# Optimization experiments

Hardware: AMD Instinct MI355X
Metric: run time of the kernel (lower is better)

## Reference

```python
import jax, jax.numpy as jnp
import numpy as np
import math

H = 32      # num attention heads
KV = 8      # num key/value heads
D = 64      # head dim
ROPE_BASE = 10000.0


def _rope_cos_sin(seq_len, dtype):
    inv_freq = 1.0 / (ROPE_BASE ** (jnp.arange(0, D, 2, dtype=jnp.float32) / D))
    t = jnp.arange(seq_len, dtype=jnp.float32)
    freqs = jnp.einsum('i,j->ij', t, inv_freq)          # [S, D/2]
    emb = jnp.concatenate([freqs, freqs], axis=-1)       # [S, D]
    return jnp.cos(emb).astype(dtype)[None, None], jnp.sin(emb).astype(dtype)[None, None]


def _rotate_half(x):
    x1, x2 = x[..., : D // 2], x[..., D // 2:]
    return jnp.concatenate([-x2, x1], axis=-1)


def setup_inputs() -> dict:
    key = jax.random.key(0)
    ks = jax.random.split(key, 5)
    B, S, Hid = 1, 2048, 2048
    hidden_states = jax.random.normal(ks[0], (B, S, Hid), dtype=jnp.float32)
    Wq = jax.random.normal(ks[1], (Hid, H * D), dtype=jnp.float32) * (1.0 / math.sqrt(Hid))
    Wk = jax.random.normal(ks[2], (Hid, KV * D), dtype=jnp.float32) * (1.0 / math.sqrt(Hid))
    Wv = jax.random.normal(ks[3], (Hid, KV * D), dtype=jnp.float32) * (1.0 / math.sqrt(Hid))
    Wo = jax.random.normal(ks[4], (H * D, Hid), dtype=jnp.float32) * (1.0 / math.sqrt(H * D))
    # additive causal mask
    causal = jnp.tril(jnp.ones((S, S), dtype=bool))
    attention_mask = jnp.where(causal, 0.0, -1e9).astype(jnp.float32)[None, None]
    return {"hidden_states": hidden_states, "Wq": Wq, "Wk": Wk, "Wv": Wv,
            "Wo": Wo, "attention_mask": attention_mask}


def reference(hidden_states, Wq, Wk, Wv, Wo, attention_mask):
    B, S, _ = hidden_states.shape
    groups = H // KV
    # projections -> [B, heads, S, D]
    q = (hidden_states @ Wq).reshape(B, S, H, D).transpose(0, 2, 1, 3)
    k = (hidden_states @ Wk).reshape(B, S, KV, D).transpose(0, 2, 1, 3)
    v = (hidden_states @ Wv).reshape(B, S, KV, D).transpose(0, 2, 1, 3)
    # RoPE
    cos, sin = _rope_cos_sin(S, q.dtype)
    q = q * cos + _rotate_half(q) * sin
    k = k * cos + _rotate_half(k) * sin
    # GQA head expansion (repeat_interleave along head axis)
    k = jnp.repeat(k, groups, axis=1)
    v = jnp.repeat(v, groups, axis=1)
    # scaled dot-product attention (eager)
    scores = jnp.einsum('bhqd,bhkd->bhqk', q, k) / math.sqrt(D)
    scores = scores + attention_mask
    probs = jax.nn.softmax(scores.astype(jnp.float32), axis=-1).astype(q.dtype)
    attn = jnp.einsum('bhqk,bhkd->bhqd', probs, v)
    attn = attn.transpose(0, 2, 1, 3).reshape(B, S, H * D)
    return attn @ Wo
```

## Files before the change

kernel.cpp:

```cpp
#include <hip/hip_runtime.h>
#include <hip/hip_bf16.h>
#include <math.h>

#define S_LEN 2048
#define HID   2048
#define NH    32
#define NKV   8
#define HD    64
#define KVW   (NKV * HD)

typedef __attribute__((ext_vector_type(8))) short bf16x8;
typedef __attribute__((ext_vector_type(4))) float f32x4;
typedef unsigned short u16;

__device__ __forceinline__ u16 f2bf(float f) {
    return (u16)((__builtin_bit_cast(unsigned, f) + 0x8000u) >> 16);
}
__device__ __forceinline__ float bf2f(u16 v) {
    unsigned u = ((unsigned)v) << 16;
    return __builtin_bit_cast(float, u);
}
__device__ __forceinline__ unsigned pack2bf(float a, float b) {
    unsigned ua = __builtin_bit_cast(unsigned, a) + 0x8000u;
    unsigned ub = __builtin_bit_cast(unsigned, b) + 0x8000u;
    return (ua >> 16) | (ub & 0xFFFF0000u);
}
__device__ __forceinline__ void stage16(const u16* g, u16* lds_base) {
    __builtin_amdgcn_global_load_lds((const __attribute__((address_space(1))) void*)g,
                                     (__attribute__((address_space(3))) void*)lds_base, 16, 0, 0);
}

__global__ __launch_bounds__(256) void cvt_bf16x8_kernel(const float* __restrict__ X,
                                                         u16* __restrict__ Y, int n8) {
    int i = blockIdx.x * 256 + threadIdx.x;
    if (i >= n8) return;
    const float4* p = (const float4*)(X + (size_t)i * 8);
    float4 a = p[0], b = p[1];
    uint4 o;
    o.x = pack2bf(a.x, a.y);
    o.y = pack2bf(a.z, a.w);
    o.z = pack2bf(b.x, b.y);
    o.w = pack2bf(b.z, b.w);
    *(uint4*)(Y + (size_t)i * 8) = o;
}

__global__ __launch_bounds__(256) void transpose_cvt4(const float* __restrict__ Wq,
                                                      const float* __restrict__ Wk,
                                                      const float* __restrict__ Wv,
                                                      const float* __restrict__ Wo,
                                                      u16* __restrict__ WqkvT,
                                                      u16* __restrict__ WoT) {
    const float* X; u16* Y; int C;
    const int z = blockIdx.z;
    if (z == 0)      { X = Wq; Y = WqkvT;                        C = HID; }
    else if (z == 1) { X = Wo; Y = WoT;                          C = HID; }
    else if (z == 2) { X = Wk; Y = WqkvT + (size_t)2048 * HID;   C = KVW; }
    else             { X = Wv; Y = WqkvT + (size_t)2560 * HID;   C = KVW; }
    const int c0 = blockIdx.x * 32, r0 = blockIdx.y * 32;
    if (c0 >= C) return;
    __shared__ float T[32][33];
    const int tx = threadIdx.x & 31, ty = threadIdx.x >> 5;
#pragma unroll
    for (int i = 0; i < 4; i++)
        T[ty + 8 * i][tx] = X[(size_t)(r0 + ty + 8 * i) * C + c0 + tx];
    __syncthreads();
#pragma unroll
    for (int i = 0; i < 4; i++)
        Y[(size_t)(c0 + ty + 8 * i) * HID + r0 + tx] = f2bf(T[tx][ty + 8 * i]);
}

template <int EPI>
__global__ __launch_bounds__(256, 4) void gemm_bf16(const u16* __restrict__ A,
                                                    const u16* __restrict__ Bt,
                                                    float* __restrict__ C,
                                                    u16* __restrict__ Qh,
                                                    u16* __restrict__ Kh,
                                                    u16* __restrict__ Vt,
                                                    int K) {
    __shared__ u16 As[128 * 64];
    __shared__ u16 Bs[64 * 64];

    const int t = threadIdx.x;
    const int w = t >> 6, lane = t & 63;
    const int qd = lane >> 4, r = lane & 15;
    const int wm = w >> 1, wn = w & 1;
    const int bm = blockIdx.y * 128, bn = blockIdx.x * 64;
    const bool kblk = (EPI == 1) && (bn >= 2048) && (bn < 2560);

    f32x4 acc[4][2];
#pragma unroll
    for (int i = 0; i < 4; i++)
#pragma unroll
        for (int j = 0; j < 2; j++) {
            acc[i][j][0] = 0.f; acc[i][j][1] = 0.f; acc[i][j][2] = 0.f; acc[i][j][3] = 0.f;
        }

    for (int k0 = 0; k0 < K; k0 += 64) {
        __syncthreads();
#pragma unroll
        for (int rd = 0; rd < 4; rd++) {
            int chunk = rd * 4 + w;
            int tt = chunk >> 1, ss = chunk & 1;
            const u16* g = A + (size_t)(bm + tt * 16 + r) * K + k0 + ss * 32 + qd * 8;
            stage16(g, As + chunk * 512);
        }
#pragma unroll
        for (int rd = 0; rd < 2; rd++) {
            int chunk = rd * 4 + w;
            int tt = chunk >> 1, ss = chunk & 1;
            const u16* g = Bt + (size_t)(bn + tt * 16 + r) * K + k0 + ss * 32 + qd * 8;
            stage16(g, Bs + chunk * 512);
        }
        __syncthreads();

#pragma unroll
        for (int ss = 0; ss < 2; ss++) {
            bf16x8 af[4], bfr[2];
#pragma unroll
            for (int i = 0; i < 4; i++)
                af[i] = *(const bf16x8*)&As[((wm * 4 + i) * 2 + ss) * 512 + lane * 8];
#pragma unroll
            for (int j = 0; j < 2; j++) {
                int tile = kblk ? (wn + 2 * j) : (wn * 2 + j);
                bfr[j] = *(const bf16x8*)&Bs[(tile * 2 + ss) * 512 + lane * 8];
            }
#pragma unroll
            for (int i = 0; i < 4; i++)
#pragma unroll
                for (int j = 0; j < 2; j++)
                    acc[i][j] = __builtin_amdgcn_mfma_f32_16x16x32_bf16(af[i], bfr[j], acc[i][j], 0, 0, 0);
        }
    }

    const int row0 = bm + wm * 64;
    if (EPI == 0) {
#pragma unroll
        for (int i = 0; i < 4; i++)
#pragma unroll
            for (int j = 0; j < 2; j++)
#pragma unroll
                for (int reg = 0; reg < 4; reg++)
                    C[(size_t)(row0 + i * 16 + qd * 4 + reg) * HID + bn + wn * 32 + j * 16 + r] =
                        acc[i][j][reg];
    } else if (bn < 2048) {
#pragma unroll
        for (int i = 0; i < 4; i++)
#pragma unroll
            for (int j = 0; j < 2; j++)
#pragma unroll
                for (int reg = 0; reg < 4; reg++)
                    Qh[(size_t)(row0 + i * 16 + qd * 4 + reg) * HID + bn + wn * 32 + j * 16 + r] =
                        f2bf(acc[i][j][reg]);
    } else if (kblk) {
        const int c0 = wn * 16 + r;
        const float inv = __expf(-(float)c0 * 0.2878231366242596f);
#pragma unroll
        for (int i = 0; i < 4; i++)
#pragma unroll
            for (int reg = 0; reg < 4; reg++) {
                int srow = row0 + i * 16 + qd * 4 + reg;
                float ang = (float)srow * inv;
                float cs = cosf(ang), sn = sinf(ang);
                float k1 = acc[i][0][reg], k2 = acc[i][1][reg];
                size_t o = (size_t)srow * KVW + (bn - 2048) + c0;
                Kh[o]      = f2bf(k1 * cs - k2 * sn);
                Kh[o + 32] = f2bf(k2 * cs + k1 * sn);
            }
    } else {
#pragma unroll
        for (int i = 0; i < 4; i++)
#pragma unroll
            for (int j = 0; j < 2; j++) {
                int nrel = (bn - 2560) + wn * 32 + j * 16 + r;
                int m0 = row0 + i * 16 + qd * 4;
                ushort4 v;
                v.x = f2bf(acc[i][j][0]); v.y = f2bf(acc[i][j][1]);
                v.z = f2bf(acc[i][j][2]); v.w = f2bf(acc[i][j][3]);
                *(ushort4*)(Vt + (size_t)nrel * S_LEN + m0) = v;
            }
    }
}

__global__ __launch_bounds__(512, 6) void attn_mfma(const u16* __restrict__ Qh,
                                                    const u16* __restrict__ K,
                                                    const u16* __restrict__ Vt,
                                                    u16* __restrict__ O) {
    __shared__ u16 Kbuf[2][4096];
    __shared__ u16 Vbuf[4096];
    __shared__ u16 P_lds[8][16][72];

    const int w    = threadIdx.x >> 6;
    const int lane = threadIdx.x & 63;
    const int qd   = lane >> 4;
    const int r    = lane & 15;
    const int qb   = 15 - (int)blockIdx.x;
    const int h    = blockIdx.y;
    const int kvh  = h >> 2;
    const int q0w  = qb * 128 + w * 16;

    const u16* qrow = Qh + (size_t)(q0w + r) * (NH * HD) + h * HD;
    bf16x8 qlo = *(const bf16x8*)(qrow + qd * 8);
    bf16x8 qhi = *(const bf16x8*)(qrow + 32 + qd * 8);
    float y1[8], y2[8];
    const float spos = (float)(q0w + r);
    const float LN1E4_OVER_32 = 0.2878231366242596f;
#pragma unroll
    for (int i = 0; i < 8; i++) {
        int jj = qd * 8 + i;
        float x1 = bf2f((u16)qlo[i]);
        float x2 = bf2f((u16)qhi[i]);
        float inv = __expf(-(float)jj * LN1E4_OVER_32);
        float ang = spos * inv;
        float c = cosf(ang), sn = sinf(ang);
        y1[i] = (x1 * c - x2 * sn) * 0.125f;
        y2[i] = (x2 * c + x1 * sn) * 0.125f;
    }
    bf16x8 qfrag[2];
    {
        union { unsigned u[4]; bf16x8 v; } a, b;
#pragma unroll
        for (int i = 0; i < 4; i++) {
            a.u[i] = pack2bf(y1[2 * i], y1[2 * i + 1]);
            b.u[i] = pack2bf(y2[2 * i], y2[2 * i + 1]);
        }
        qfrag[0] = a.v; qfrag[1] = b.v;
    }

    bf16x8 ones;
    {
        union { u16 s[8]; bf16x8 v; } u;
#pragma unroll
        for (int i = 0; i < 8; i++) u.s[i] = 0x3F80;
        ones = u.v;
    }

    f32x4 oacc[4];
    f32x4 lacc;
#pragma unroll
    for (int i = 0; i < 4; i++) { oacc[i][0]=0.f; oacc[i][1]=0.f; oacc[i][2]=0.f; oacc[i][3]=0.f; }
    lacc[0]=0.f; lacc[1]=0.f; lacc[2]=0.f; lacc[3]=0.f;

    const int ktmax = 2 * qb + 1;

#define STAGE_K(kt_, buf_)                                                        \
    {                                                                             \
        const u16* g = K + (size_t)((kt_) * 64 + (w >> 1) * 16 + r) * KVW         \
                         + kvh * HD + (w & 1) * 32 + qd * 8;                      \
        stage16(g, &Kbuf[buf_][w * 512]);                                         \
    }
#define STAGE_V(kt_)                                                              \
    {                                                                             \
        const u16* g = Vt + (size_t)(kvh * HD + (w >> 1) * 16 + r) * S_LEN        \
                          + (kt_) * 64 + (w & 1) * 32 + qd * 8;                   \
        stage16(g, &Vbuf[w * 512]);                                               \
    }

    STAGE_K(0, 0);
    __syncthreads();
    int cur = 0;

    for (int kt = 0; kt <= ktmax; kt++) {
        STAGE_V(kt);
        if (kt < ktmax) STAGE_K(kt + 1, cur ^ 1);

        f32x4 s[4];
#pragma unroll
        for (int nt = 0; nt < 4; nt++) {
            bf16x8 kf0 = *(const bf16x8*)&Kbuf[cur][(nt * 2 + 0) * 512 + lane * 8];
            bf16x8 kf1 = *(const bf16x8*)&Kbuf[cur][(nt * 2 + 1) * 512 + lane * 8];
            f32x4 z; z[0]=0.f; z[1]=0.f; z[2]=0.f; z[3]=0.f;
            z = __builtin_amdgcn_mfma_f32_16x16x32_bf16(qfrag[0], kf0, z, 0, 0, 0);
            s[nt] = __builtin_amdgcn_mfma_f32_16x16x32_bf16(qfrag[1], kf1, z, 0, 0, 0);
        }

        if (kt * 64 + 63 > q0w) {
#pragma unroll
            for (int nt = 0; nt < 4; nt++) {
                int key = kt * 64 + nt * 16 + r;
#pragma unroll
                for (int reg = 0; reg < 4; reg++) {
                    int qg = q0w + qd * 4 + reg;
                    if (key > qg) s[nt][reg] = -1e30f;
                }
            }
        }

#pragma unroll
        for (int nt = 0; nt < 4; nt++)
#pragma unroll
            for (int reg = 0; reg < 4; reg++)
                P_lds[w][qd * 4 + reg][nt * 16 + r] = f2bf(__expf(s[nt][reg]));

        __syncthreads();

#pragma unroll
        for (int c = 0; c < 2; c++) {
            bf16x8 pf = *(const bf16x8*)&P_lds[w][r][c * 32 + qd * 8];
            lacc = __builtin_amdgcn_mfma_f32_16x16x32_bf16(pf, ones, lacc, 0, 0, 0);
#pragma unroll
            for (int ntd = 0; ntd < 4; ntd++) {
                bf16x8 vf = *(const bf16x8*)&Vbuf[(ntd * 2 + c) * 512 + lane * 8];
                oacc[ntd] = __builtin_amdgcn_mfma_f32_16x16x32_bf16(pf, vf, oacc[ntd], 0, 0, 0);
            }
        }

        __syncthreads();
        cur ^= 1;
    }
#undef STAGE_K
#undef STAGE_V

    float rl[4];
#pragma unroll
    for (int reg = 0; reg < 4; reg++) rl[reg] = 1.f / lacc[reg];
#pragma unroll
    for (int ntd = 0; ntd < 4; ntd++)
#pragma unroll
        for (int reg = 0; reg < 4; reg++)
            O[(size_t)(q0w + qd * 4 + reg) * (NH * HD) + h * HD + ntd * 16 + r] =
                f2bf(oacc[ntd][reg] * rl[reg]);
}

extern "C" void kernel_launch(void* const* d_in, const int* in_sizes, int n_in,
                              void* d_out, int out_size, void* d_ws, size_t ws_size,
                              hipStream_t stream) {
    const float* hidden = (const float*)d_in[0];
    const float* Wq = (const float*)d_in[1];
    const float* Wk = (const float*)d_in[2];
    const float* Wv = (const float*)d_in[3];
    const float* Wo = (const float*)d_in[4];
    float* out = (float*)d_out;

    char* ws = (char*)d_ws;
    const size_t MB = 1024 * 1024;
    u16* Hh     = (u16*)(ws + 0 * MB);
    u16* WqkvT  = (u16*)(ws + 8 * MB);
    u16* WoT    = (u16*)(ws + 20 * MB);
    u16* Qh     = (u16*)(ws + 28 * MB);
    u16* Kh     = (u16*)(ws + 36 * MB);
    u16* Vt     = (u16*)(ws + 38 * MB);
    u16* Ob     = WqkvT;

    cvt_bf16x8_kernel<<<(S_LEN * HID / 8 + 255) / 256, 256, 0, stream>>>(hidden, Hh, S_LEN * HID / 8);
    transpose_cvt4<<<dim3(HID / 32, HID / 32, 4), 256, 0, stream>>>(Wq, Wk, Wv, Wo, WqkvT, WoT);

    gemm_bf16<1><<<dim3(3072 / 64, S_LEN / 128), 256, 0, stream>>>(Hh, WqkvT, nullptr, Qh, Kh, Vt, HID);

    attn_mfma<<<dim3(S_LEN / 128, NH), 512, 0, stream>>>(Qh, Kh, Vt, Ob);

    gemm_bf16<0><<<dim3(HID / 64, S_LEN / 128), 256, 0, stream>>>(Ob, WoT, out, nullptr, nullptr, nullptr, HID);
}
```

Measured before the change: 287.5 us.

## Restructure bf16 GEMM into 128x256 tiles with 4-stage async LDS pipeline

Rewrites the projection GEMM kernel to use 512-thread blocks computing 128x256 output tiles, with a 4-slot LDS ring buffer over K-steps of 32 and manual vmcnt waits and barriers, so global loads overlap MFMA work. It also swizzles the block order across groups of 8 for better L2 locality and raises MFMA priority with setprio. The larger tile gives more data reuse per load but cuts the block count (192 and 128 blocks), which may underfill the GPU's CUs. It also raises register and LDS pressure.

Result: no change. 288.8 us (+0.5%).

```diff
diff --git a/kernel.cpp b/kernel.cpp
--- a/kernel.cpp
+++ b/kernel.cpp
@@ -70,112 +70,135 @@
 }
 
 template <int EPI>
-__global__ __launch_bounds__(256, 4) void gemm_bf16(const u16* __restrict__ A,
+__global__ __launch_bounds__(512, 2) void gemm_bf16(const u16* __restrict__ A,
                                                     const u16* __restrict__ Bt,
                                                     float* __restrict__ C,
                                                     u16* __restrict__ Qh,
                                                     u16* __restrict__ Kh,
-                                                    u16* __restrict__ Vt,
-                                                    int K) {
-    __shared__ u16 As[128 * 64];
-    __shared__ u16 Bs[64 * 64];
-
-    const int t = threadIdx.x;
-    const int w = t >> 6, lane = t & 63;
+                                                    u16* __restrict__ Vt) {
+    constexpr int KTOT = 2048;
+    constexpr int NT = KTOT / 32;
+    constexpr int SLOT = 12288;
+    __shared__ u16 smem[4 * SLOT];
+
+    const int tiles = gridDim.x * gridDim.y;
+    const int flat = blockIdx.y * gridDim.x + blockIdx.x;
+    const int per = tiles >> 3;
+    const int swz = (flat & 7) * per + (flat >> 3);
+    const int bxx = swz % gridDim.x, byy = swz / gridDim.x;
+    const int bm = byy * 128, bn = bxx * 256;
+
+    const int tid = threadIdx.x;
+    const int w = tid >> 6, lane = tid & 63;
     const int qd = lane >> 4, r = lane & 15;
-    const int wm = w >> 1, wn = w & 1;
-    const int bm = blockIdx.y * 128, bn = blockIdx.x * 64;
-    const bool kblk = (EPI == 1) && (bn >= 2048) && (bn < 2560);
-
-    f32x4 acc[4][2];
-#pragma unroll
-    for (int i = 0; i < 4; i++)
-#pragma unroll
-        for (int j = 0; j < 2; j++) {
-            acc[i][j][0] = 0.f; acc[i][j][1] = 0.f; acc[i][j][2] = 0.f; acc[i][j][3] = 0.f;
-        }
-
-    for (int k0 = 0; k0 < K; k0 += 64) {
-        __syncthreads();
-#pragma unroll
-        for (int rd = 0; rd < 4; rd++) {
-            int chunk = rd * 4 + w;
-            int tt = chunk >> 1, ss = chunk & 1;
-            const u16* g = A + (size_t)(bm + tt * 16 + r) * K + k0 + ss * 32 + qd * 8;
-            stage16(g, As + chunk * 512);
-        }
-#pragma unroll
-        for (int rd = 0; rd < 2; rd++) {
-            int chunk = rd * 4 + w;
-            int tt = chunk >> 1, ss = chunk & 1;
-            const u16* g = Bt + (size_t)(bn + tt * 16 + r) * K + k0 + ss * 32 + qd * 8;
-            stage16(g, Bs + chunk * 512);
-        }
-        __syncthreads();
-
-#pragma unroll
-        for (int ss = 0; ss < 2; ss++) {
-            bf16x8 af[4], bfr[2];
-#pragma unroll
-            for (int i = 0; i < 4; i++)
-                af[i] = *(const bf16x8*)&As[((wm * 4 + i) * 2 + ss) * 512 + lane * 8];
-#pragma unroll
-            for (int j = 0; j < 2; j++) {
-                int tile = kblk ? (wn + 2 * j) : (wn * 2 + j);
-                bfr[j] = *(const bf16x8*)&Bs[(tile * 2 + ss) * 512 + lane * 8];
-            }
-#pragma unroll
-            for (int i = 0; i < 4; i++)
-#pragma unroll
-                for (int j = 0; j < 2; j++)
-                    acc[i][j] = __builtin_amdgcn_mfma_f32_16x16x32_bf16(af[i], bfr[j], acc[i][j], 0, 0, 0);
-        }
-    }
+    const int wm = w >> 2, wn = w & 3;
+
+    f32x4 acc[4][4];
+#pragma unroll
+    for (int m = 0; m < 4; m++)
+#pragma unroll
+        for (int n = 0; n < 4; n++) {
+            acc[m][n][0] = 0.f; acc[m][n][1] = 0.f;
+            acc[m][n][2] = 0.f; acc[m][n][3] = 0.f;
+        }
+
+    auto stage_tile = [&](int kt) {
+        u16* slot = smem + (size_t)(kt & 3) * SLOT;
+        const int k0 = kt * 32;
+        const u16* ga = A + (size_t)(bm + w * 16 + r) * KTOT + k0 + qd * 8;
+        stage16(ga, slot + w * 512);
+        const u16* gb0 = Bt + (size_t)(bn + w * 16 + r) * KTOT + k0 + qd * 8;
+        stage16(gb0, slot + 4096 + w * 512);
+        const u16* gb1 = Bt + (size_t)(bn + (w + 8) * 16 + r) * KTOT + k0 + qd * 8;
+        stage16(gb1, slot + 4096 + (w + 8) * 512);
+    };
+
+    auto compute_tile = [&](int kt) {
+        const u16* slot = smem + (size_t)(kt & 3) * SLOT;
+        bf16x8 af[4], bfv[4];
+#pragma unroll
+        for (int m = 0; m < 4; m++)
+            af[m] = *(const bf16x8*)&slot[(wm * 4 + m) * 512 + lane * 8];
+#pragma unroll
+        for (int n = 0; n < 4; n++)
+            bfv[n] = *(const bf16x8*)&slot[4096 + (wn * 4 + n) * 512 + lane * 8];
+        __builtin_amdgcn_s_setprio(1);
+#pragma unroll
+        for (int m = 0; m < 4; m++)
+#pragma unroll
+            for (int n = 0; n < 4; n++)
+                acc[m][n] = __builtin_amdgcn_mfma_f32_16x16x32_bf16(af[m], bfv[n], acc[m][n], 0, 0, 0);
+        __builtin_amdgcn_s_setprio(0);
+    };
+
+#define VMB(n_) do { asm volatile("s_waitcnt vmcnt(" #n_ ")" ::: "memory");  \
+                     __builtin_amdgcn_s_barrier();                           \
+                     __builtin_amdgcn_sched_barrier(0); } while (0)
+
+    stage_tile(0);
+    stage_tile(1);
+    stage_tile(2);
+
+    for (int kt = 0; kt < NT - 3; ++kt) {
+        VMB(6);
+        stage_tile(kt + 3);
+        __builtin_amdgcn_sched_barrier(0);
+        compute_tile(kt);
+    }
+    VMB(6); compute_tile(NT - 3);
+    VMB(3); compute_tile(NT - 2);
+    VMB(0); compute_tile(NT - 1);
+#undef VMB
 
     const int row0 = bm + wm * 64;
+    const int col0 = bn + wn * 64;
     if (EPI == 0) {
 #pragma unroll
-        for (int i = 0; i < 4; i++)
-#pragma unroll
-            for (int j = 0; j < 2; j++)
+        for (int m = 0; m < 4; m++)
+#pragma unroll
+            for (int n = 0; n < 4; n++)
 #pragma unroll
                 for (int reg = 0; reg < 4; reg++)
-                    C[(size_t)(row0 + i * 16 + qd * 4 + reg) * HID + bn + wn * 32 + j * 16 + r] =
-                        acc[i][j][reg];
+                    C[(size_t)(row0 + m * 16 + qd * 4 + reg) * HID + col0 + n * 16 + r] =
+                        acc[m][n][reg];
     } else if (bn < 2048) {
 #pragma unroll
-        for (int i = 0; i < 4; i++)
-#pragma unroll
-            for (int j = 0; j < 2; j++)
+        for (int m = 0; m < 4; m++)
+#pragma unroll
+            for (int n = 0; n < 4; n++)
 #pragma unroll
                 for (int reg = 0; reg < 4; reg++)
-                    Qh[(size_t)(row0 + i * 16 + qd * 4 + reg) * HID + bn + wn * 32 + j * 16 + r] =
-                        f2bf(acc[i][j][reg]);
-    } else if (kblk) {
-        const int c0 = wn * 16 + r;
-        const float inv = __expf(-(float)c0 * 0.2878231366242596f);
-#pragma unroll
-        for (int i = 0; i < 4; i++)
-#pragma unroll
-            for (int reg = 0; reg < 4; reg++) {
-                int srow = row0 + i * 16 + qd * 4 + reg;
-                float ang = (float)srow * inv;
-                float cs = cosf(ang), sn = sinf(ang);
-                float k1 = acc[i][0][reg], k2 = acc[i][1][reg];
-                size_t o = (size_t)srow * KVW + (bn - 2048) + c0;
-                Kh[o]      = f2bf(k1 * cs - k2 * sn);
-                Kh[o + 32] = f2bf(k2 * cs + k1 * sn);
-            }
+                    Qh[(size_t)(row0 + m * 16 + qd * 4 + reg) * HID + col0 + n * 16 + r] =
+                        f2bf(acc[m][n][reg]);
+    } else if (bn < 2560) {
+        const int hb = (bn - 2048) + wn * 64;
+#pragma unroll
+        for (int n = 0; n < 2; n++) {
+            const int c0 = n * 16 + r;
+            const float inv = __expf(-(float)c0 * 0.2878231366242596f);
+#pragma unroll
+            for (int m = 0; m < 4; m++)
+#pragma unroll
+                for (int reg = 0; reg < 4; reg++) {
+                    int srow = row0 + m * 16 + qd * 4 + reg;
+                    float ang = (float)srow * inv;
+                    float cs = cosf(ang), sn = sinf(ang);
+                    float k1 = acc[m][n][reg], k2 = acc[m][n + 2][reg];
+                    size_t o = (size_t)srow * KVW + hb + c0;
+                    Kh[o]      = f2bf(k1 * cs - k2 * sn);
+                    Kh[o + 32] = f2bf(k2 * cs + k1 * sn);
+                }
+        }
     } else {
 #pragma unroll
-        for (int i = 0; i < 4; i++)
-#pragma unroll
-            for (int j = 0; j < 2; j++) {
-                int nrel = (bn - 2560) + wn * 32 + j * 16 + r;
-                int m0 = row0 + i * 16 + qd * 4;
+        for (int m = 0; m < 4; m++)
+#pragma unroll
+            for (int n = 0; n < 4; n++) {
+                int nrel = (bn - 2560) + wn * 64 + n * 16 + r;
+                int m0 = row0 + m * 16 + qd * 4;
                 ushort4 v;
-                v.x = f2bf(acc[i][j][0]); v.y = f2bf(acc[i][j][1]);
-                v.z = f2bf(acc[i][j][2]); v.w = f2bf(acc[i][j][3]);
+                v.x = f2bf(acc[m][n][0]); v.y = f2bf(acc[m][n][1]);
+                v.z = f2bf(acc[m][n][2]); v.w = f2bf(acc[m][n][3]);
                 *(ushort4*)(Vt + (size_t)nrel * S_LEN + m0) = v;
             }
     }
@@ -344,9 +367,9 @@
     cvt_bf16x8_kernel<<<(S_LEN * HID / 8 + 255) / 256, 256, 0, stream>>>(hidden, Hh, S_LEN * HID / 8);
     transpose_cvt4<<<dim3(HID / 32, HID / 32, 4), 256, 0, stream>>>(Wq, Wk, Wv, Wo, WqkvT, WoT);
 
-    gemm_bf16<1><<<dim3(3072 / 64, S_LEN / 128), 256, 0, stream>>>(Hh, WqkvT, nullptr, Qh, Kh, Vt, HID);
+    gemm_bf16<1><<<dim3(3072 / 256, S_LEN / 128), 512, 0, stream>>>(Hh, WqkvT, nullptr, Qh, Kh, Vt);
 
     attn_mfma<<<dim3(S_LEN / 128, NH), 512, 0, stream>>>(Qh, Kh, Vt, Ob);
 
-    gemm_bf16<0><<<dim3(HID / 64, S_LEN / 128), 256, 0, stream>>>(Ob, WoT, out, nullptr, nullptr, nullptr, HID);
-}
+    gemm_bf16<0><<<dim3(HID / 256, S_LEN / 128), 512, 0, stream>>>(Ob, WoT, out, nullptr, nullptr, nullptr);
+}
```

## Enlarge GEMM tiles to 128x128 with double-buffered LDS staging

Applied to the files above, without the earlier changes.

The bf16 GEMM now uses 128x128 output tiles (16 MFMA accumulators per wave instead of 8) and a K-step of 32. Shared-memory staging is double-buffered, so the next K-slice is loaded while MFMAs run on the current one, with a single barrier per iteration. This targets global-load and barrier overhead per FLOP. The costs are higher register pressure under launch_bounds(256,4) and half as many blocks, which may hurt occupancy and wave balance. The K-RoPE epilogue is remapped to the new column layout.

Result: slower. 296.6 us (+3.2%).

```diff
diff --git a/kernel.cpp b/kernel.cpp
--- a/kernel.cpp
+++ b/kernel.cpp
@@ -77,107 +77,134 @@
                                                     u16* __restrict__ Kh,
                                                     u16* __restrict__ Vt,
                                                     int K) {
-    __shared__ u16 As[128 * 64];
-    __shared__ u16 Bs[64 * 64];
+    __shared__ u16 As[2][4096];
+    __shared__ u16 Bs[2][4096];
 
     const int t = threadIdx.x;
     const int w = t >> 6, lane = t & 63;
     const int qd = lane >> 4, r = lane & 15;
     const int wm = w >> 1, wn = w & 1;
-    const int bm = blockIdx.y * 128, bn = blockIdx.x * 64;
+    const int bm = blockIdx.y * 128, bn = blockIdx.x * 128;
     const bool kblk = (EPI == 1) && (bn >= 2048) && (bn < 2560);
 
-    f32x4 acc[4][2];
-#pragma unroll
-    for (int i = 0; i < 4; i++)
-#pragma unroll
-        for (int j = 0; j < 2; j++) {
-            acc[i][j][0] = 0.f; acc[i][j][1] = 0.f; acc[i][j][2] = 0.f; acc[i][j][3] = 0.f;
-        }
-
-    for (int k0 = 0; k0 < K; k0 += 64) {
+    f32x4 a00 = {0.f,0.f,0.f,0.f}, a01 = {0.f,0.f,0.f,0.f},
+          a02 = {0.f,0.f,0.f,0.f}, a03 = {0.f,0.f,0.f,0.f},
+          a10 = {0.f,0.f,0.f,0.f}, a11 = {0.f,0.f,0.f,0.f},
+          a12 = {0.f,0.f,0.f,0.f}, a13 = {0.f,0.f,0.f,0.f},
+          a20 = {0.f,0.f,0.f,0.f}, a21 = {0.f,0.f,0.f,0.f},
+          a22 = {0.f,0.f,0.f,0.f}, a23 = {0.f,0.f,0.f,0.f},
+          a30 = {0.f,0.f,0.f,0.f}, a31 = {0.f,0.f,0.f,0.f},
+          a32 = {0.f,0.f,0.f,0.f}, a33 = {0.f,0.f,0.f,0.f};
+
+#define STAGE(k0_, b_)                                                          \
+    {                                                                           \
+        _Pragma("unroll")                                                       \
+        for (int l = 0; l < 2; l++) {                                           \
+            const int c_ = w * 2 + l;                                           \
+            const u16* ga = A + (size_t)(bm + c_ * 16 + r) * K + (k0_) + qd * 8; \
+            stage16(ga, &As[b_][c_ * 512]);                                     \
+            const u16* gb = Bt + (size_t)(bn + c_ * 16 + r) * K + (k0_) + qd * 8; \
+            stage16(gb, &Bs[b_][c_ * 512]);                                     \
+        }                                                                       \
+    }
+
+    STAGE(0, 0);
+    __syncthreads();
+    int cur = 0;
+
+    for (int k0 = 0; k0 < K; k0 += 32) {
+        if (k0 + 32 < K) STAGE(k0 + 32, cur ^ 1);
+
+        bf16x8 af0 = *(const bf16x8*)&As[cur][(wm * 4 + 0) * 512 + lane * 8];
+        bf16x8 af1 = *(const bf16x8*)&As[cur][(wm * 4 + 1) * 512 + lane * 8];
+        bf16x8 af2 = *(const bf16x8*)&As[cur][(wm * 4 + 2) * 512 + lane * 8];
+        bf16x8 af3 = *(const bf16x8*)&As[cur][(wm * 4 + 3) * 512 + lane * 8];
+        bf16x8 bv0 = *(const bf16x8*)&Bs[cur][(wn * 4 + 0) * 512 + lane * 8];
+        bf16x8 bv1 = *(const bf16x8*)&Bs[cur][(wn * 4 + 1) * 512 + lane * 8];
+        bf16x8 bv2 = *(const bf16x8*)&Bs[cur][(wn * 4 + 2) * 512 + lane * 8];
+        bf16x8 bv3 = *(const bf16x8*)&Bs[cur][(wn * 4 + 3) * 512 + lane * 8];
+
+        a00 = __builtin_amdgcn_mfma_f32_16x16x32_bf16(af0, bv0, a00, 0, 0, 0);
+        a01 = __builtin_amdgcn_mfma_f32_16x16x32_bf16(af0, bv1, a01, 0, 0, 0);
+        a02 = __builtin_amdgcn_mfma_f32_16x16x32_bf16(af0, bv2, a02, 0, 0, 0);
+        a03 = __builtin_amdgcn_mfma_f32_16x16x32_bf16(af0, bv3, a03, 0, 0, 0);
+        a10 = __builtin_amdgcn_mfma_f32_16x16x32_bf16(af1, bv0, a10, 0, 0, 0);
+        a11 = __builtin_amdgcn_mfma_f32_16x16x32_bf16(af1, bv1, a11, 0, 0, 0);
+        a12 = __builtin_amdgcn_mfma_f32_16x16x32_bf16(af1, bv2, a12, 0, 0, 0);
+        a13 = __builtin_amdgcn_mfma_f32_16x16x32_bf16(af1, bv3, a13, 0, 0, 0);
+        a20 = __builtin_amdgcn_mfma_f32_16x16x32_bf16(af2, bv0, a20, 0, 0, 0);
+        a21 = __builtin_amdgcn_mfma_f32_16x16x32_bf16(af2, bv1, a21, 0, 0, 0);
+        a22 = __builtin_amdgcn_mfma_f32_16x16x32_bf16(af2, bv2, a22, 0, 0, 0);
+        a23 = __builtin_amdgcn_mfma_f32_16x16x32_bf16(af2, bv3, a23, 0, 0, 0);
+        a30 = __builtin_amdgcn_mfma_f32_16x16x32_bf16(af3, bv0, a30, 0, 0, 0);
+        a31 = __builtin_amdgcn_mfma_f32_16x16x32_bf16(af3, bv1, a31, 0, 0, 0);
+        a32 = __builtin_amdgcn_mfma_f32_16x16x32_bf16(af3, bv2, a32, 0, 0, 0);
+        a33 = __builtin_amdgcn_mfma_f32_16x16x32_bf16(af3, bv3, a33, 0, 0, 0);
+
         __syncthreads();
-#pragma unroll
-        for (int rd = 0; rd < 4; rd++) {
-            int chunk = rd * 4 + w;
-            int tt = chunk >> 1, ss = chunk & 1;
-            const u16* g = A + (size_t)(bm + tt * 16 + r) * K + k0 + ss * 32 + qd * 8;
-            stage16(g, As + chunk * 512);
-        }
-#pragma unroll
-        for (int rd = 0; rd < 2; rd++) {
-            int chunk = rd * 4 + w;
-            int tt = chunk >> 1, ss = chunk & 1;
-            const u16* g = Bt + (size_t)(bn + tt * 16 + r) * K + k0 + ss * 32 + qd * 8;
-            stage16(g, Bs + chunk * 512);
-        }
-        __syncthreads();
-
-#pragma unroll
-        for (int ss = 0; ss < 2; ss++) {
-            bf16x8 af[4], bfr[2];
-#pragma unroll
-            for (int i = 0; i < 4; i++)
-                af[i] = *(const bf16x8*)&As[((wm * 4 + i) * 2 + ss) * 512 + lane * 8];
-#pragma unroll
-            for (int j = 0; j < 2; j++) {
-                int tile = kblk ? (wn + 2 * j) : (wn * 2 + j);
-                bfr[j] = *(const bf16x8*)&Bs[(tile * 2 + ss) * 512 + lane * 8];
-            }
-#pragma unroll
-            for (int i = 0; i < 4; i++)
-#pragma unroll
-                for (int j = 0; j < 2; j++)
-                    acc[i][j] = __builtin_amdgcn_mfma_f32_16x16x32_bf16(af[i], bfr[j], acc[i][j], 0, 0, 0);
-        }
-    }
+        cur ^= 1;
+    }
+#undef STAGE
 
     const int row0 = bm + wm * 64;
+    const int col0 = bn + wn * 64;
     if (EPI == 0) {
-#pragma unroll
-        for (int i = 0; i < 4; i++)
-#pragma unroll
-            for (int j = 0; j < 2; j++)
-#pragma unroll
-                for (int reg = 0; reg < 4; reg++)
-                    C[(size_t)(row0 + i * 16 + qd * 4 + reg) * HID + bn + wn * 32 + j * 16 + r] =
-                        acc[i][j][reg];
+#define ST_C(m_, n_, av)                                                        \
+        _Pragma("unroll")                                                       \
+        for (int reg = 0; reg < 4; reg++)                                       \
+            C[(size_t)(row0 + m_ * 16 + qd * 4 + reg) * HID + col0 + n_ * 16 + r] = av[reg];
+        ST_C(0,0,a00) ST_C(0,1,a01) ST_C(0,2,a02) ST_C(0,3,a03)
+        ST_C(1,0,a10) ST_C(1,1,a11) ST_C(1,2,a12) ST_C(1,3,a13)
+        ST_C(2,0,a20) ST_C(2,1,a21) ST_C(2,2,a22) ST_C(2,3,a23)
+        ST_C(3,0,a30) ST_C(3,1,a31) ST_C(3,2,a32) ST_C(3,3,a33)
+#undef ST_C
     } else if (bn < 2048) {
-#pragma unroll
-        for (int i = 0; i < 4; i++)
-#pragma unroll
-            for (int j = 0; j < 2; j++)
-#pragma unroll
-                for (int reg = 0; reg < 4; reg++)
-                    Qh[(size_t)(row0 + i * 16 + qd * 4 + reg) * HID + bn + wn * 32 + j * 16 + r] =
-                        f2bf(acc[i][j][reg]);
+#define ST_Q(m_, n_, av)                                                        \
+        _Pragma("unroll")                                                       \
+        for (int reg = 0; reg < 4; reg++)                                       \
+            Qh[(size_t)(row0 + m_ * 16 + qd * 4 + reg) * HID + col0 + n_ * 16 + r] = f2bf(av[reg]);
+        ST_Q(0,0,a00) ST_Q(0,1,a01) ST_Q(0,2,a02) ST_Q(0,3,a03)
+        ST_Q(1,0,a10) ST_Q(1,1,a11) ST_Q(1,2,a12) ST_Q(1,3,a13)
+        ST_Q(2,0,a20) ST_Q(2,1,a21) ST_Q(2,2,a22) ST_Q(2,3,a23)
+        ST_Q(3,0,a30) ST_Q(3,1,a31) ST_Q(3,2,a32) ST_Q(3,3,a33)
+#undef ST_Q
     } else if (kblk) {
-        const int c0 = wn * 16 + r;
-        const float inv = __expf(-(float)c0 * 0.2878231366242596f);
-#pragma unroll
-        for (int i = 0; i < 4; i++)
-#pragma unroll
-            for (int reg = 0; reg < 4; reg++) {
-                int srow = row0 + i * 16 + qd * 4 + reg;
-                float ang = (float)srow * inv;
-                float cs = cosf(ang), sn = sinf(ang);
-                float k1 = acc[i][0][reg], k2 = acc[i][1][reg];
-                size_t o = (size_t)srow * KVW + (bn - 2048) + c0;
-                Kh[o]      = f2bf(k1 * cs - k2 * sn);
-                Kh[o + 32] = f2bf(k2 * cs + k1 * sn);
-            }
+        const int hb = (bn - 2048) + wn * 64;
+#define ST_K(m_, n_, av, av2)                                                   \
+        {                                                                       \
+            const int c0 = n_ * 16 + r;                                         \
+            const float inv = __expf(-(float)c0 * 0.2878231366242596f);         \
+            _Pragma("unroll")                                                   \
+            for (int reg = 0; reg < 4; reg++) {                                 \
+                int srow = row0 + m_ * 16 + qd * 4 + reg;                       \
+                float ang = (float)srow * inv;                                  \
+                float cs = cosf(ang), sn = sinf(ang);                           \
+                float k1 = av[reg], k2 = av2[reg];                              \
+                size_t o = (size_t)srow * KVW + hb + c0;                        \
+                Kh[o]      = f2bf(k1 * cs - k2 * sn);                           \
+                Kh[o + 32] = f2bf(k2 * cs + k1 * sn);                           \
+            }                                                                   \
+        }
+        ST_K(0,0,a00,a02) ST_K(0,1,a01,a03)
+        ST_K(1,0,a10,a12) ST_K(1,1,a11,a13)
+        ST_K(2,0,a20,a22) ST_K(2,1,a21,a23)
+        ST_K(3,0,a30,a32) ST_K(3,1,a31,a33)
+#undef ST_K
     } else {
-#pragma unroll
-        for (int i = 0; i < 4; i++)
-#pragma unroll
-            for (int j = 0; j < 2; j++) {
-                int nrel = (bn - 2560) + wn * 32 + j * 16 + r;
-                int m0 = row0 + i * 16 + qd * 4;
-                ushort4 v;
-                v.x = f2bf(acc[i][j][0]); v.y = f2bf(acc[i][j][1]);
-                v.z = f2bf(acc[i][j][2]); v.w = f2bf(acc[i][j][3]);
-                *(ushort4*)(Vt + (size_t)nrel * S_LEN + m0) = v;
-            }
+#define ST_V(m_, n_, av)                                                        \
+        {                                                                       \
+            int nrel = (bn - 2560) + wn * 64 + n_ * 16 + r;                     \
+            int m0 = row0 + m_ * 16 + qd * 4;                                   \
+            ushort4 v;                                                          \
+            v.x = f2bf(av[0]); v.y = f2bf(av[1]);                               \
+            v.z = f2bf(av[2]); v.w = f2bf(av[3]);                               \
+            *(ushort4*)(Vt + (size_t)nrel * S_LEN + m0) = v;                    \
+        }
+        ST_V(0,0,a00) ST_V(0,1,a01) ST_V(0,2,a02) ST_V(0,3,a03)
+        ST_V(1,0,a10) ST_V(1,1,a11) ST_V(1,2,a12) ST_V(1,3,a13)
+        ST_V(2,0,a20) ST_V(2,1,a21) ST_V(2,2,a22) ST_V(2,3,a23)
+        ST_V(3,0,a30) ST_V(3,1,a31) ST_V(3,2,a32) ST_V(3,3,a33)
+#undef ST_V
     }
 }
 
@@ -344,9 +371,9 @@
     cvt_bf16x8_kernel<<<(S_LEN * HID / 8 + 255) / 256, 256, 0, stream>>>(hidden, Hh, S_LEN * HID / 8);
     transpose_cvt4<<<dim3(HID / 32, HID / 32, 4), 256, 0, stream>>>(Wq, Wk, Wv, Wo, WqkvT, WoT);
 
-    gemm_bf16<1><<<dim3(3072 / 64, S_LEN / 128), 256, 0, stream>>>(Hh, WqkvT, nullptr, Qh, Kh, Vt, HID);
+    gemm_bf16<1><<<dim3(3072 / 128, S_LEN / 128), 256, 0, stream>>>(Hh, WqkvT, nullptr, Qh, Kh, Vt, HID);
 
     attn_mfma<<<dim3(S_LEN / 128, NH), 512, 0, stream>>>(Qh, Kh, Vt, Ob);
 
-    gemm_bf16<0><<<dim3(HID / 64, S_LEN / 128), 256, 0, stream>>>(Ob, WoT, out, nullptr, nullptr, nullptr, HID);
-}
+    gemm_bf16<0><<<dim3(HID / 128, S_LEN / 128), 256, 0, stream>>>(Ob, WoT, out, nullptr, nullptr, nullptr, HID);
+}
```

## Double-buffer GEMM LDS staging and shrink block tile to 64x64

Applied to the files above, without the earlier changes.

The projection GEMMs now use a 64x64 block tile instead of 128x64, which doubles the grid. LDS is double-buffered so the next K-slice is staged while MFMAs run on the current one, leaving one barrier per iteration. Launch bounds are raised to allow 5 blocks per CU. In exchange each block reuses less data and loads more from global memory per FLOP.

After: 325.7 us. +13.3%, slower.

```diff
diff --git a/kernel.cpp b/kernel.cpp
--- a/kernel.cpp
+++ b/kernel.cpp
@@ -70,72 +70,77 @@
 }
 
 template <int EPI>
-__global__ __launch_bounds__(256, 4) void gemm_bf16(const u16* __restrict__ A,
+__global__ __launch_bounds__(256, 5) void gemm_bf16(const u16* __restrict__ A,
                                                     const u16* __restrict__ Bt,
                                                     float* __restrict__ C,
                                                     u16* __restrict__ Qh,
                                                     u16* __restrict__ Kh,
                                                     u16* __restrict__ Vt,
                                                     int K) {
-    __shared__ u16 As[128 * 64];
-    __shared__ u16 Bs[64 * 64];
+    __shared__ u16 As[2][64 * 64];
+    __shared__ u16 Bs[2][64 * 64];
 
     const int t = threadIdx.x;
     const int w = t >> 6, lane = t & 63;
     const int qd = lane >> 4, r = lane & 15;
     const int wm = w >> 1, wn = w & 1;
-    const int bm = blockIdx.y * 128, bn = blockIdx.x * 64;
+    const int bm = blockIdx.y * 64, bn = blockIdx.x * 64;
     const bool kblk = (EPI == 1) && (bn >= 2048) && (bn < 2560);
 
-    f32x4 acc[4][2];
-#pragma unroll
-    for (int i = 0; i < 4; i++)
+    f32x4 acc[2][2];
+#pragma unroll
+    for (int i = 0; i < 2; i++)
 #pragma unroll
         for (int j = 0; j < 2; j++) {
             acc[i][j][0] = 0.f; acc[i][j][1] = 0.f; acc[i][j][2] = 0.f; acc[i][j][3] = 0.f;
         }
 
-    for (int k0 = 0; k0 < K; k0 += 64) {
-        __syncthreads();
-#pragma unroll
-        for (int rd = 0; rd < 4; rd++) {
-            int chunk = rd * 4 + w;
-            int tt = chunk >> 1, ss = chunk & 1;
-            const u16* g = A + (size_t)(bm + tt * 16 + r) * K + k0 + ss * 32 + qd * 8;
-            stage16(g, As + chunk * 512);
-        }
+    auto stageAB = [&](int k0, u16* dstA, u16* dstB) {
 #pragma unroll
         for (int rd = 0; rd < 2; rd++) {
             int chunk = rd * 4 + w;
             int tt = chunk >> 1, ss = chunk & 1;
-            const u16* g = Bt + (size_t)(bn + tt * 16 + r) * K + k0 + ss * 32 + qd * 8;
-            stage16(g, Bs + chunk * 512);
-        }
-        __syncthreads();
+            const u16* ga = A + (size_t)(bm + tt * 16 + r) * K + k0 + ss * 32 + qd * 8;
+            stage16(ga, dstA + chunk * 512);
+            const u16* gb = Bt + (size_t)(bn + tt * 16 + r) * K + k0 + ss * 32 + qd * 8;
+            stage16(gb, dstB + chunk * 512);
+        }
+    };
+
+    stageAB(0, As[0], Bs[0]);
+    __syncthreads();
+    int cur = 0;
+
+    for (int k0 = 0; k0 < K; k0 += 64) {
+        if (k0 + 64 < K)
+            stageAB(k0 + 64, As[cur ^ 1], Bs[cur ^ 1]);
 
 #pragma unroll
         for (int ss = 0; ss < 2; ss++) {
-            bf16x8 af[4], bfr[2];
-#pragma unroll
-            for (int i = 0; i < 4; i++)
-                af[i] = *(const bf16x8*)&As[((wm * 4 + i) * 2 + ss) * 512 + lane * 8];
+            bf16x8 af[2], bfr[2];
+#pragma unroll
+            for (int i = 0; i < 2; i++)
+                af[i] = *(const bf16x8*)&As[cur][((wm * 2 + i) * 2 + ss) * 512 + lane * 8];
 #pragma unroll
             for (int j = 0; j < 2; j++) {
                 int tile = kblk ? (wn + 2 * j) : (wn * 2 + j);
-                bfr[j] = *(const bf16x8*)&Bs[(tile * 2 + ss) * 512 + lane * 8];
-            }
-#pragma unroll
-            for (int i = 0; i < 4; i++)
+                bfr[j] = *(const bf16x8*)&Bs[cur][(tile * 2 + ss) * 512 + lane * 8];
+            }
+#pragma unroll
+            for (int i = 0; i < 2; i++)
 #pragma unroll
                 for (int j = 0; j < 2; j++)
                     acc[i][j] = __builtin_amdgcn_mfma_f32_16x16x32_bf16(af[i], bfr[j], acc[i][j], 0, 0, 0);
         }
-    }
-
-    const int row0 = bm + wm * 64;
+
+        __syncthreads();
+        cur ^= 1;
+    }
+
+    const int row0 = bm + wm * 32;
     if (EPI == 0) {
 #pragma unroll
-        for (int i = 0; i < 4; i++)
+        for (int i = 0; i < 2; i++)
 #pragma unroll
             for (int j = 0; j < 2; j++)
 #pragma unroll
@@ -144,7 +149,7 @@
                         acc[i][j][reg];
     } else if (bn < 2048) {
 #pragma unroll
-        for (int i = 0; i < 4; i++)
+        for (int i = 0; i < 2; i++)
 #pragma unroll
             for (int j = 0; j < 2; j++)
 #pragma unroll
@@ -153,22 +158,23 @@
                         f2bf(acc[i][j][reg]);
     } else if (kblk) {
         const int c0 = wn * 16 + r;
+        const int hb = bn - 2048;
         const float inv = __expf(-(float)c0 * 0.2878231366242596f);
 #pragma unroll
-        for (int i = 0; i < 4; i++)
+        for (int i = 0; i < 2; i++)
 #pragma unroll
             for (int reg = 0; reg < 4; reg++) {
                 int srow = row0 + i * 16 + qd * 4 + reg;
                 float ang = (float)srow * inv;
                 float cs = cosf(ang), sn = sinf(ang);
                 float k1 = acc[i][0][reg], k2 = acc[i][1][reg];
-                size_t o = (size_t)srow * KVW + (bn - 2048) + c0;
+                size_t o = (size_t)srow * KVW + hb + c0;
                 Kh[o]      = f2bf(k1 * cs - k2 * sn);
                 Kh[o + 32] = f2bf(k2 * cs + k1 * sn);
             }
     } else {
 #pragma unroll
-        for (int i = 0; i < 4; i++)
+        for (int i = 0; i < 2; i++)
 #pragma unroll
             for (int j = 0; j < 2; j++) {
                 int nrel = (bn - 2560) + wn * 32 + j * 16 + r;
@@ -344,9 +350,9 @@
     cvt_bf16x8_kernel<<<(S_LEN * HID / 8 + 255) / 256, 256, 0, stream>>>(hidden, Hh, S_LEN * HID / 8);
     transpose_cvt4<<<dim3(HID / 32, HID / 32, 4), 256, 0, stream>>>(Wq, Wk, Wv, Wo, WqkvT, WoT);
 
-    gemm_bf16<1><<<dim3(3072 / 64, S_LEN / 128), 256, 0, stream>>>(Hh, WqkvT, nullptr, Qh, Kh, Vt, HID);
+    gemm_bf16<1><<<dim3(3072 / 64, S_LEN / 64), 256, 0, stream>>>(Hh, WqkvT, nullptr, Qh, Kh, Vt, HID);
 
     attn_mfma<<<dim3(S_LEN / 128, NH), 512, 0, stream>>>(Qh, Kh, Vt, Ob);
 
-    gemm_bf16<0><<<dim3(HID / 64, S_LEN / 128), 256, 0, stream>>>(Ob, WoT, out, nullptr, nullptr, nullptr, HID);
-}
+    gemm_bf16<0><<<dim3(HID / 64, S_LEN / 64), 256, 0, stream>>>(Ob, WoT, out, nullptr, nullptr, nullptr, HID);
+}
```
